# Kernel tuning notes

Hardware: AMD Instinct MI355X
Metric: run time of the kernel (lower is better)

The kernel has to match this reference:

```python
import jax, jax.numpy as jnp
import numpy as np

D = 1024  # in_features == latent_dim
EPS = 1e-5


def _layernorm(x, g, b):
    mu = jnp.mean(x, axis=-1, keepdims=True)
    var = jnp.mean(jnp.square(x - mu), axis=-1, keepdims=True)
    return (x - mu) * jax.lax.rsqrt(var + EPS) * g + b


def setup_inputs() -> dict:
    key = jax.random.key(0)
    ks = jax.random.split(key, 8)
    s = 1.0 / np.sqrt(D)
    return {
        "x": jax.random.normal(ks[0], (4, 4096, D), dtype=jnp.float32),
        "w_qkv": jax.random.uniform(ks[1], (3 * D, D), jnp.float32, -s, s),
        "w_o": jax.random.uniform(ks[2], (D, D), jnp.float32, -s, s),
        "w1": jax.random.uniform(ks[3], (D, D), jnp.float32, -s, s),
        "b1": jax.random.uniform(ks[4], (D,), jnp.float32, -s, s),
        "w2": jax.random.uniform(ks[5], (D, D), jnp.float32, -s, s),
        "b2": jax.random.uniform(ks[6], (D,), jnp.float32, -s, s),
        "ln1_g": jnp.ones((D,), jnp.float32),
        "ln1_b": jnp.zeros((D,), jnp.float32),
        "ln2_g": jnp.ones((D,), jnp.float32),
        "ln2_b": jnp.zeros((D,), jnp.float32),
    }


def reference(x, w_qkv, w_o, w1, b1, w2, b2, ln1_g, ln1_b, ln2_g, ln2_b):
    B, S, _ = x.shape
    scale = 1.0 / np.sqrt(D * 1)  # 1/sqrt(latent_dim * n_heads), n_heads=1
    qkv = jnp.einsum("bsd,ed->bse", x, w_qkv)            # [B,S,3D]
    qkv = qkv.reshape(B, S, 1, 3 * D).transpose(0, 2, 1, 3)  # [B,1,S,3D]
    q, k, v = jnp.split(qkv, 3, axis=-1)                  # each [B,1,S,D]
    logits = jnp.einsum("bhid,bhjd->bhij", q, k) * scale  # [B,1,S,S]
    # Faithful quirk: softmax over the HEAD axis (dim=1). With 1 head this
    # yields an all-ones attention matrix.
    attn = jax.nn.softmax(logits, axis=1)
    vals = jnp.einsum("bhij,bhjd->bhid", attn, v)         # [B,1,S,D]
    vals = vals.transpose(0, 2, 1, 3).reshape(B, S, D)
    attn_out = jnp.einsum("bsd,ed->bse", vals, w_o)
    # squeeze(-2) is a no-op for S>1
    x = _layernorm(x + attn_out, ln1_g, ln1_b)
    h = jax.nn.gelu(jnp.einsum("bsd,ed->bse", x, w1) + b1, approximate=False)
    mlp_out = jnp.einsum("bsd,ed->bse", h, w2) + b2
    return _layernorm(x + mlp_out, ln2_g, ln2_b)
```

## Files before the change

kernel.cpp:

```cpp
#include <hip/hip_runtime.h>
#include <hip/hip_bf16.h>

typedef __hip_bfloat16 bf16;
typedef __attribute__((ext_vector_type(8))) short short8;
typedef __attribute__((ext_vector_type(4))) float f32x4;

#define DDIM 1024
#define SEQ  4096
#define NB   4
#define MTOT (NB*SEQ)

static __device__ __forceinline__ unsigned short f2bf(float f) {
    __hip_bfloat16 h = __float2bfloat16(f);
    unsigned short u; __builtin_memcpy(&u, &h, 2); return u;
}
static __device__ __forceinline__ float bf2f(unsigned short u) {
    __hip_bfloat16 h; __builtin_memcpy(&h, &u, 2); return __bfloat162float(h);
}

__global__ __launch_bounds__(256) void cast_w_kernel(
    const float* __restrict__ w1, const float* __restrict__ w2,
    unsigned short* __restrict__ w1b, unsigned short* __restrict__ w2b)
{
    size_t idx = ((size_t)blockIdx.x*256 + threadIdx.x) * 4;
    float4 a = *(const float4*)(w1 + idx);
    ushort4 o; o.x=f2bf(a.x); o.y=f2bf(a.y); o.z=f2bf(a.z); o.w=f2bf(a.w);
    *(ushort4*)(w1b + idx) = o;
    float4 b = *(const float4*)(w2 + idx);
    o.x=f2bf(b.x); o.y=f2bf(b.y); o.z=f2bf(b.z); o.w=f2bf(b.w);
    *(ushort4*)(w2b + idx) = o;
}

__global__ __launch_bounds__(256) void colsum_partial_kernel(
    const float* __restrict__ x, float* __restrict__ partial)
{
    int d  = blockIdx.x*256 + threadIdx.x;
    int b  = blockIdx.y;
    int sl = blockIdx.z;
    const float* p = x + ((size_t)b*SEQ + (size_t)sl*128)*DDIM + d;
    float s = 0.f;
    #pragma unroll 4
    for (int i = 0; i < 128; ++i) s += p[(size_t)i*DDIM];
    partial[((size_t)sl*NB + b)*DDIM + d] = s;
}

__global__ __launch_bounds__(256) void colsum_reduce_kernel(
    const float* __restrict__ partial, float* __restrict__ xsum)
{
    int d = blockIdx.x*256 + threadIdx.x;
    int b = blockIdx.y;
    float s = 0.f;
    #pragma unroll
    for (int sl = 0; sl < 32; ++sl) s += partial[((size_t)sl*NB + b)*DDIM + d];
    xsum[b*DDIM + d] = s;
}

__global__ __launch_bounds__(256) void matvec_kernel(
    const float* __restrict__ W, const float* __restrict__ vin, float* __restrict__ vout)
{
    int b = blockIdx.y;
    int g = threadIdx.x >> 4;
    int t = threadIdx.x & 15;
    int e = blockIdx.x*16 + g;
    const float* w = W + (size_t)e*DDIM;
    const float* v = vin + b*DDIM;
    float s = 0.f;
    for (int k = t; k < DDIM; k += 16) s += w[k]*v[k];
    #pragma unroll
    for (int o = 8; o; o >>= 1) s += __shfl_down(s, o, 16);
    if (t == 0) vout[b*DDIM + e] = s;
}

__global__ __launch_bounds__(256) void ln1_kernel(
    const float* __restrict__ x, const float* __restrict__ avec,
    const float* __restrict__ g1, const float* __restrict__ b1,
    unsigned short* __restrict__ x1b)
{
    int row = blockIdx.x;
    int b   = row >> 12;
    int tid = threadIdx.x;
    const float4* xr = (const float4*)(x + (size_t)row*DDIM);
    const float4* av = (const float4*)(avec + (size_t)b*DDIM);
    float4 xv = xr[tid], a4 = av[tid];
    float y0 = xv.x+a4.x, y1 = xv.y+a4.y, y2 = xv.z+a4.z, y3 = xv.w+a4.w;
    float s  = y0+y1+y2+y3;
    float ss = y0*y0+y1*y1+y2*y2+y3*y3;
    #pragma unroll
    for (int o = 32; o; o >>= 1) { s += __shfl_down(s,o,64); ss += __shfl_down(ss,o,64); }
    __shared__ float red[8];
    if ((tid&63) == 0) { red[tid>>6] = s; red[4+(tid>>6)] = ss; }
    __syncthreads();
    float St = red[0]+red[1]+red[2]+red[3];
    float Sq = red[4]+red[5]+red[6]+red[7];
    float mu = St*(1.0f/DDIM);
    float rs = rsqrtf(Sq*(1.0f/DDIM) - mu*mu + 1e-5f);
    float4 g4 = ((const float4*)g1)[tid];
    float4 bb = ((const float4*)b1)[tid];
    ushort4 o;
    o.x = f2bf((y0-mu)*rs*g4.x + bb.x);
    o.y = f2bf((y1-mu)*rs*g4.y + bb.y);
    o.z = f2bf((y2-mu)*rs*g4.z + bb.z);
    o.w = f2bf((y3-mu)*rs*g4.w + bb.w);
    *(ushort4*)(x1b + (size_t)row*DDIM + tid*4) = o;
}

__global__ __launch_bounds__(256, 4) void gemm_bk32_kernel(
    const bf16* __restrict__ A, const bf16* __restrict__ Bw,
    const float* __restrict__ bias, unsigned short* __restrict__ outb)
{
    constexpr int K = 1024, N = 1024, BK = 32, NT = K / BK;
    __shared__ __align__(16) bf16 lds[2][2][128*BK];
    const int tid  = threadIdx.x;
    const int wave = tid >> 6, lane = tid & 63;

    int bid = blockIdx.x;
    int swz = (bid & 7) * 128 + (bid >> 3);
    const size_t bm = (size_t)(swz >> 3) * 128;
    const size_t bn = (size_t)(swz & 7) * 128;

    const int wr = (wave >> 1) * 64, wc = (wave & 1) * 64;
    const int fr = lane & 15, fs = lane >> 4;

    const int srow = tid >> 2;
    const int sk   = (((tid & 3) ^ ((tid >> 3) & 3)) << 3);

    const int swo = (fs ^ ((fr >> 1) & 3)) << 4;

    f32x4 acc[4][4] = {};
    const bf16* Ab = A  + bm * K;
    const bf16* Bb = Bw + bn * K;

    auto stage = [&](int b, int kt) {
        #pragma unroll
        for (int mat = 0; mat < 2; ++mat) {
            const bf16* src = (mat == 0 ? Ab : Bb);
            #pragma unroll
            for (int g = 0; g < 2; ++g) {
                const bf16* gp = src + (size_t)(g*64 + srow) * K + kt*BK + sk;
                __builtin_amdgcn_global_load_lds(
                    (const __attribute__((address_space(1))) void*)gp,
                    (__attribute__((address_space(3))) void*)
                        ((char*)&lds[b][mat][0] + g*4096 + wave*1024),
                    16, 0, 0);
            }
        }
    };

    stage(0, 0);

    #pragma unroll 2
    for (int t = 0; t < NT; ++t) {
        const int cur = t & 1;
        if (t < NT-1) {
            stage(cur ^ 1, t + 1);
            asm volatile("s_waitcnt vmcnt(4)" ::: "memory");
        } else {
            asm volatile("s_waitcnt vmcnt(0)" ::: "memory");
        }
        __builtin_amdgcn_s_barrier();

        const char* LA = (const char*)&lds[cur][0][0];
        const char* LB = (const char*)&lds[cur][1][0];
        short8 af[4], bfr[4];
        #pragma unroll
        for (int m = 0; m < 4; ++m) af[m]  = *(const short8*)(LA + (wr + m*16 + fr)*64 + swo);
        #pragma unroll
        for (int n = 0; n < 4; ++n) bfr[n] = *(const short8*)(LB + (wc + n*16 + fr)*64 + swo);
        __builtin_amdgcn_s_setprio(1);
        #pragma unroll
        for (int m = 0; m < 4; ++m)
            #pragma unroll
            for (int n = 0; n < 4; ++n)
                acc[m][n] = __builtin_amdgcn_mfma_f32_16x16x32_bf16(af[m], bfr[n], acc[m][n], 0, 0, 0);
        __builtin_amdgcn_s_setprio(0);
        __builtin_amdgcn_s_barrier();
    }

    const int crow = fs * 4;
    #pragma unroll
    for (int n = 0; n < 4; ++n) {
        size_t col = bn + wc + n*16 + fr;
        float bv = bias[col];
        #pragma unroll
        for (int m = 0; m < 4; ++m) {
            #pragma unroll
            for (int r = 0; r < 4; ++r) {
                size_t row = bm + wr + m*16 + crow + r;
                float v = acc[m][n][r] + bv;
                float ge = 0.5f*v*(1.0f + erff(v*0.70710678118f));
                outb[row*(size_t)N + col] = f2bf(ge);
            }
        }
    }
}

__global__ __launch_bounds__(256, 2) void gemm2_kernel(
    const bf16* __restrict__ A, const bf16* __restrict__ Bw,
    const float* __restrict__ bias, unsigned short* __restrict__ xy,
    float2* __restrict__ part)
{
    constexpr int K = 1024, N = 1024, BK = 64, NT = K / BK;
    __shared__ __align__(16) bf16 lds[2][2][128*BK];
    const int tid  = threadIdx.x;
    const int wave = tid >> 6, lane = tid & 63;

    int bid = blockIdx.x;
    int swz = (bid & 7) * 128 + (bid >> 3);
    const size_t bm = (size_t)(swz >> 3) * 128;
    const size_t bn = (size_t)(swz & 7) * 128;

    const int wm = wave >> 1;
    const int wn = wave & 1;

    const int srow = tid >> 3;
    const int skel = (((tid & 7) ^ ((tid >> 3) & 7)) << 3);

    const int fr = lane & 15;
    const int fs = lane >> 4;
    int foff[2];
    #pragma unroll
    for (int ks = 0; ks < 2; ++ks)
        foff[ks] = fr*128 + (((ks*4 + fs) ^ (fr & 7)) << 4);

    f32x4 acc[4][4] = {};
    const bf16* Ab = A  + bm * K;
    const bf16* Bb = Bw + bn * K;

    auto stage = [&](int b, int kt) {
        #pragma unroll
        for (int mat = 0; mat < 2; ++mat) {
            const bf16* src = (mat == 0 ? Ab : Bb);
            #pragma unroll
            for (int g = 0; g < 4; ++g) {
                int row = g*32 + srow;
                const bf16* gp = src + (size_t)row * K + kt*BK + skel;
                __builtin_amdgcn_global_load_lds(
                    (const __attribute__((address_space(1))) void*)gp,
                    (__attribute__((address_space(3))) void*)
                        ((char*)&lds[b][mat][0] + g*4096 + wave*1024),
                    16, 0, 0);
            }
        }
    };

    stage(0, 0);

    #pragma unroll 2
    for (int t = 0; t < NT; ++t) {
        const int cur = t & 1;
        if (t < NT-1) {
            stage(cur ^ 1, t + 1);
            asm volatile("s_waitcnt vmcnt(8)" ::: "memory");
        } else {
            asm volatile("s_waitcnt vmcnt(0)" ::: "memory");
        }
        __builtin_amdgcn_s_barrier();

        const char* LA = (const char*)&lds[cur][0][0] + wm*8192;
        const char* LB = (const char*)&lds[cur][1][0] + wn*8192;
        #pragma unroll
        for (int ks = 0; ks < 2; ++ks) {
            short8 af[4], bfr[4];
            #pragma unroll
            for (int m = 0; m < 4; ++m) af[m]  = *(const short8*)(LA + m*2048 + foff[ks]);
            #pragma unroll
            for (int n = 0; n < 4; ++n) bfr[n] = *(const short8*)(LB + n*2048 + foff[ks]);
            __builtin_amdgcn_s_setprio(1);
            #pragma unroll
            for (int m = 0; m < 4; ++m)
                #pragma unroll
                for (int n = 0; n < 4; ++n)
                    acc[m][n] = __builtin_amdgcn_mfma_f32_16x16x32_bf16(
                        af[m], bfr[n], acc[m][n], 0, 0, 0);
            __builtin_amdgcn_s_setprio(0);
        }
        __builtin_amdgcn_s_barrier();
    }

    float vs[4][4] = {}, vq[4][4] = {};
    #pragma unroll
    for (int n = 0; n < 4; ++n) {
        size_t col = bn + wn*64 + n*16 + fr;
        float bv = bias[col];
        #pragma unroll
        for (int m = 0; m < 4; ++m) {
            #pragma unroll
            for (int r = 0; r < 4; ++r) {
                size_t row = bm + wm*64 + m*16 + fs*4 + r;
                size_t idx = row*(size_t)N + col;
                float v = acc[m][n][r] + bv + bf2f(xy[idx]);
                unsigned short qb = f2bf(v);
                xy[idx] = qb;
                float vv = bf2f(qb);
                vs[m][r] += vv;
                vq[m][r] += vv*vv;
            }
        }
    }
    #pragma unroll
    for (int o = 1; o < 16; o <<= 1) {
        #pragma unroll
        for (int m = 0; m < 4; ++m)
            #pragma unroll
            for (int r = 0; r < 4; ++r) {
                vs[m][r] += __shfl_xor(vs[m][r], o);
                vq[m][r] += __shfl_xor(vq[m][r], o);
            }
    }
    float* lred = (float*)&lds[0][0][0];
    if (fr == 0) {
        #pragma unroll
        for (int m = 0; m < 4; ++m)
            #pragma unroll
            for (int r = 0; r < 4; ++r) {
                int rl = wm*64 + m*16 + fs*4 + r;
                lred[(wn*128 + rl)*2]     = vs[m][r];
                lred[(wn*128 + rl)*2 + 1] = vq[m][r];
            }
    }
    __syncthreads();
    if (tid < 128) {
        float s  = lred[tid*2]       + lred[(128 + tid)*2];
        float sq = lred[tid*2 + 1]   + lred[(128 + tid)*2 + 1];
        part[(bm + tid)*8 + (bn >> 7)] = make_float2(s, sq);
    }
}

__global__ __launch_bounds__(256) void ln2_apply_kernel(
    const unsigned short* __restrict__ yb, const float2* __restrict__ part,
    const float* __restrict__ g2, const float* __restrict__ b2,
    float* __restrict__ out)
{
    int row = blockIdx.x;
    int tid = threadIdx.x;
    float s = 0.f, sq = 0.f;
    #pragma unroll
    for (int i = 0; i < 8; ++i) {
        float2 p = part[(size_t)row*8 + i];
        s += p.x; sq += p.y;
    }
    float mu = s * (1.0f/DDIM);
    float rs = rsqrtf(sq * (1.0f/DDIM) - mu*mu + 1e-5f);
    ushort4 yv = *(const ushort4*)(yb + (size_t)row*DDIM + tid*4);
    float4 g4 = ((const float4*)g2)[tid];
    float4 bb = ((const float4*)b2)[tid];
    float4 o;
    o.x = (bf2f(yv.x) - mu)*rs*g4.x + bb.x;
    o.y = (bf2f(yv.y) - mu)*rs*g4.y + bb.y;
    o.z = (bf2f(yv.z) - mu)*rs*g4.z + bb.z;
    o.w = (bf2f(yv.w) - mu)*rs*g4.w + bb.w;
    ((float4*)(out + (size_t)row*DDIM))[tid] = o;
}

extern "C" void kernel_launch(void* const* d_in, const int* in_sizes, int n_in,
                              void* d_out, int out_size, void* d_ws, size_t ws_size,
                              hipStream_t stream)
{
    const float* x     = (const float*)d_in[0];
    const float* w_qkv = (const float*)d_in[1];
    const float* w_o   = (const float*)d_in[2];
    const float* w1    = (const float*)d_in[3];
    const float* b1    = (const float*)d_in[4];
    const float* w2    = (const float*)d_in[5];
    const float* b2    = (const float*)d_in[6];
    const float* ln1g  = (const float*)d_in[7];
    const float* ln1b  = (const float*)d_in[8];
    const float* ln2g  = (const float*)d_in[9];
    const float* ln2b  = (const float*)d_in[10];
    float* out = (float*)d_out;
    char* ws = (char*)d_ws;

    unsigned short* x1b = (unsigned short*)(ws);
    unsigned short* hb  = (unsigned short*)(ws + 33554432);
    unsigned short* w1b = (unsigned short*)(ws + 67108864);
    unsigned short* w2b = (unsigned short*)(ws + 69206016);
    float* partial = (float*)(ws + 71303168);
    float* xsum    = (float*)(ws + 71827456);
    float* tvec    = (float*)(ws + 71843840);
    float* avec    = (float*)(ws + 71860224);
    float2* lnpart = (float2*)(ws + 67108864);

    cast_w_kernel<<<dim3(1024), 256, 0, stream>>>(w1, w2, w1b, w2b);
    colsum_partial_kernel<<<dim3(4, NB, 32), 256, 0, stream>>>(x, partial);
    colsum_reduce_kernel<<<dim3(4, NB), 256, 0, stream>>>(partial, xsum);
    matvec_kernel<<<dim3(64, NB), 256, 0, stream>>>(w_qkv + (size_t)2*DDIM*DDIM, xsum, tvec);
    matvec_kernel<<<dim3(64, NB), 256, 0, stream>>>(w_o, tvec, avec);
    ln1_kernel<<<dim3(MTOT), 256, 0, stream>>>(x, avec, ln1g, ln1b, x1b);
    gemm_bk32_kernel<<<dim3(1024), 256, 0, stream>>>(
        (const bf16*)x1b, (const bf16*)w1b, b1, hb);
    gemm2_kernel<<<dim3(1024), 256, 0, stream>>>(
        (const bf16*)hb, (const bf16*)w2b, b2, x1b, lnpart);
    ln2_apply_kernel<<<dim3(MTOT), 256, 0, stream>>>(x1b, lnpart, ln2g, ln2b, out);
}
```

Measured before the change: 173.0 us.

## Merge weight cast with column-sum kernel and deepen GEMM1 K-tile to 64

Result: no change. 171.3 us (-1.0%).

```diff
diff --git a/kernel.cpp b/kernel.cpp
--- a/kernel.cpp
+++ b/kernel.cpp
@@ -18,30 +18,30 @@
     __hip_bfloat16 h; __builtin_memcpy(&h, &u, 2); return __bfloat162float(h);
 }
 
-__global__ __launch_bounds__(256) void cast_w_kernel(
+__global__ __launch_bounds__(256) void prep_kernel(
     const float* __restrict__ w1, const float* __restrict__ w2,
-    unsigned short* __restrict__ w1b, unsigned short* __restrict__ w2b)
-{
-    size_t idx = ((size_t)blockIdx.x*256 + threadIdx.x) * 4;
-    float4 a = *(const float4*)(w1 + idx);
-    ushort4 o; o.x=f2bf(a.x); o.y=f2bf(a.y); o.z=f2bf(a.z); o.w=f2bf(a.w);
-    *(ushort4*)(w1b + idx) = o;
-    float4 b = *(const float4*)(w2 + idx);
-    o.x=f2bf(b.x); o.y=f2bf(b.y); o.z=f2bf(b.z); o.w=f2bf(b.w);
-    *(ushort4*)(w2b + idx) = o;
-}
-
-__global__ __launch_bounds__(256) void colsum_partial_kernel(
+    unsigned short* __restrict__ w1b, unsigned short* __restrict__ w2b,
     const float* __restrict__ x, float* __restrict__ partial)
 {
-    int d  = blockIdx.x*256 + threadIdx.x;
-    int b  = blockIdx.y;
-    int sl = blockIdx.z;
-    const float* p = x + ((size_t)b*SEQ + (size_t)sl*128)*DDIM + d;
-    float s = 0.f;
-    #pragma unroll 4
-    for (int i = 0; i < 128; ++i) s += p[(size_t)i*DDIM];
-    partial[((size_t)sl*NB + b)*DDIM + d] = s;
+    int bid = blockIdx.x;
+    if (bid < 1024) {
+        size_t idx = ((size_t)bid*256 + threadIdx.x) * 4;
+        float4 a = *(const float4*)(w1 + idx);
+        ushort4 o; o.x=f2bf(a.x); o.y=f2bf(a.y); o.z=f2bf(a.z); o.w=f2bf(a.w);
+        *(ushort4*)(w1b + idx) = o;
+        float4 b = *(const float4*)(w2 + idx);
+        o.x=f2bf(b.x); o.y=f2bf(b.y); o.z=f2bf(b.z); o.w=f2bf(b.w);
+        *(ushort4*)(w2b + idx) = o;
+    } else {
+        int idx = bid - 1024;
+        int dx = idx & 3, b = (idx >> 2) & 3, sl = idx >> 4;
+        int d  = dx*256 + threadIdx.x;
+        const float* p = x + ((size_t)b*SEQ + (size_t)sl*128)*DDIM + d;
+        float s = 0.f;
+        #pragma unroll 4
+        for (int i = 0; i < 128; ++i) s += p[(size_t)i*DDIM];
+        partial[((size_t)sl*NB + b)*DDIM + d] = s;
+    }
 }
 
 __global__ __launch_bounds__(256) void colsum_reduce_kernel(
@@ -104,11 +104,11 @@
     *(ushort4*)(x1b + (size_t)row*DDIM + tid*4) = o;
 }
 
-__global__ __launch_bounds__(256, 4) void gemm_bk32_kernel(
+__global__ __launch_bounds__(256, 2) void gemm1_kernel(
     const bf16* __restrict__ A, const bf16* __restrict__ Bw,
     const float* __restrict__ bias, unsigned short* __restrict__ outb)
 {
-    constexpr int K = 1024, N = 1024, BK = 32, NT = K / BK;
+    constexpr int K = 1024, N = 1024, BK = 64, NT = K / BK;
     __shared__ __align__(16) bf16 lds[2][2][128*BK];
     const int tid  = threadIdx.x;
     const int wave = tid >> 6, lane = tid & 63;
@@ -118,13 +118,18 @@
     const size_t bm = (size_t)(swz >> 3) * 128;
     const size_t bn = (size_t)(swz & 7) * 128;
 
-    const int wr = (wave >> 1) * 64, wc = (wave & 1) * 64;
-    const int fr = lane & 15, fs = lane >> 4;
-
-    const int srow = tid >> 2;
-    const int sk   = (((tid & 3) ^ ((tid >> 3) & 3)) << 3);
-
-    const int swo = (fs ^ ((fr >> 1) & 3)) << 4;
+    const int wm = wave >> 1;
+    const int wn = wave & 1;
+
+    const int srow = tid >> 3;
+    const int skel = (((tid & 7) ^ ((tid >> 3) & 7)) << 3);
+
+    const int fr = lane & 15;
+    const int fs = lane >> 4;
+    int foff[2];
+    #pragma unroll
+    for (int ks = 0; ks < 2; ++ks)
+        foff[ks] = fr*128 + (((ks*4 + fs) ^ (fr & 7)) << 4);
 
     f32x4 acc[4][4] = {};
     const bf16* Ab = A  + bm * K;
@@ -135,8 +140,9 @@
         for (int mat = 0; mat < 2; ++mat) {
             const bf16* src = (mat == 0 ? Ab : Bb);
             #pragma unroll
-            for (int g = 0; g < 2; ++g) {
-                const bf16* gp = src + (size_t)(g*64 + srow) * K + kt*BK + sk;
+            for (int g = 0; g < 4; ++g) {
+                int row = g*32 + srow;
+                const bf16* gp = src + (size_t)row * K + kt*BK + skel;
                 __builtin_amdgcn_global_load_lds(
                     (const __attribute__((address_space(1))) void*)gp,
                     (__attribute__((address_space(3))) void*)
@@ -153,39 +159,42 @@
         const int cur = t & 1;
         if (t < NT-1) {
             stage(cur ^ 1, t + 1);
-            asm volatile("s_waitcnt vmcnt(4)" ::: "memory");
+            asm volatile("s_waitcnt vmcnt(8)" ::: "memory");
         } else {
             asm volatile("s_waitcnt vmcnt(0)" ::: "memory");
         }
         __builtin_amdgcn_s_barrier();
 
-        const char* LA = (const char*)&lds[cur][0][0];
-        const char* LB = (const char*)&lds[cur][1][0];
-        short8 af[4], bfr[4];
-        #pragma unroll
-        for (int m = 0; m < 4; ++m) af[m]  = *(const short8*)(LA + (wr + m*16 + fr)*64 + swo);
-        #pragma unroll
-        for (int n = 0; n < 4; ++n) bfr[n] = *(const short8*)(LB + (wc + n*16 + fr)*64 + swo);
-        __builtin_amdgcn_s_setprio(1);
-        #pragma unroll
-        for (int m = 0; m < 4; ++m)
-            #pragma unroll
-            for (int n = 0; n < 4; ++n)
-                acc[m][n] = __builtin_amdgcn_mfma_f32_16x16x32_bf16(af[m], bfr[n], acc[m][n], 0, 0, 0);
-        __builtin_amdgcn_s_setprio(0);
+        const char* LA = (const char*)&lds[cur][0][0] + wm*8192;
+        const char* LB = (const char*)&lds[cur][1][0] + wn*8192;
+        #pragma unroll
+        for (int ks = 0; ks < 2; ++ks) {
+            short8 af[4], bfr[4];
+            #pragma unroll
+            for (int m = 0; m < 4; ++m) af[m]  = *(const short8*)(LA + m*2048 + foff[ks]);
+            #pragma unroll
+            for (int n = 0; n < 4; ++n) bfr[n] = *(const short8*)(LB + n*2048 + foff[ks]);
+            __builtin_amdgcn_s_setprio(1);
+            #pragma unroll
+            for (int m = 0; m < 4; ++m)
+                #pragma unroll
+                for (int n = 0; n < 4; ++n)
+                    acc[m][n] = __builtin_amdgcn_mfma_f32_16x16x32_bf16(
+                        af[m], bfr[n], acc[m][n], 0, 0, 0);
+            __builtin_amdgcn_s_setprio(0);
+        }
         __builtin_amdgcn_s_barrier();
     }
 
-    const int crow = fs * 4;
     #pragma unroll
     for (int n = 0; n < 4; ++n) {
-        size_t col = bn + wc + n*16 + fr;
+        size_t col = bn + wn*64 + n*16 + fr;
         float bv = bias[col];
         #pragma unroll
         for (int m = 0; m < 4; ++m) {
             #pragma unroll
             for (int r = 0; r < 4; ++r) {
-                size_t row = bm + wr + m*16 + crow + r;
+                size_t row = bm + wm*64 + m*16 + fs*4 + r;
                 float v = acc[m][n][r] + bv;
                 float ge = 0.5f*v*(1.0f + erff(v*0.70710678118f));
                 outb[row*(size_t)N + col] = f2bf(ge);
@@ -380,13 +389,12 @@
     float* avec    = (float*)(ws + 71860224);
     float2* lnpart = (float2*)(ws + 67108864);
 
-    cast_w_kernel<<<dim3(1024), 256, 0, stream>>>(w1, w2, w1b, w2b);
-    colsum_partial_kernel<<<dim3(4, NB, 32), 256, 0, stream>>>(x, partial);
+    prep_kernel<<<dim3(1536), 256, 0, stream>>>(w1, w2, w1b, w2b, x, partial);
     colsum_reduce_kernel<<<dim3(4, NB), 256, 0, stream>>>(partial, xsum);
     matvec_kernel<<<dim3(64, NB), 256, 0, stream>>>(w_qkv + (size_t)2*DDIM*DDIM, xsum, tvec);
     matvec_kernel<<<dim3(64, NB), 256, 0, stream>>>(w_o, tvec, avec);
     ln1_kernel<<<dim3(MTOT), 256, 0, stream>>>(x, avec, ln1g, ln1b, x1b);
-    gemm_bk32_kernel<<<dim3(1024), 256, 0, stream>>>(
+    gemm1_kernel<<<dim3(1024), 256, 0, stream>>>(
         (const bf16*)x1b, (const bf16*)w1b, b1, hb);
     gemm2_kernel<<<dim3(1024), 256, 0, stream>>>(
         (const bf16*)hb, (const bf16*)w2b, b2, x1b, lnpart);
```
